# Optimization experiments

Hardware: AMD Instinct MI355X
Metric: run time of the kernel (lower is better)

The kernel has to match this reference:

```python
import jax, jax.numpy as jnp
import numpy as np

PATCH = 7
STRIDE = 1
PDIM = 3 * PATCH * PATCH  # 147


def _extract_patches(im):
    # torch.nn.Unfold(kernel=7, stride=1): output [b, c*k*k, L] with channel-major
    # ordering, which matches conv_general_dilated_patches' channel-major layout.
    b = im.shape[0]
    p = jax.lax.conv_general_dilated_patches(
        im, filter_shape=(PATCH, PATCH), window_strides=(STRIDE, STRIDE), padding='VALID'
    )  # [b, 147, h', w']
    p = p.reshape(b, PDIM, -1).transpose(0, 2, 1)  # [b, L, 147]
    # normalize_patch='mean': std_mean over ALL dims, only the mean is subtracted
    return p - p.mean()


def setup_inputs() -> dict:
    key = jax.random.key(0)
    k1, k2, k3, k4, k5 = jax.random.split(key, 5)
    B, C, H, W = 16, 3, 128, 128
    L = ((H - PATCH) // STRIDE + 1) ** 2  # 14884
    n_samples, n_proj = 4096, 128
    x = jax.random.normal(k1, (B, C, H, W), dtype=jnp.float32)
    y = jax.random.normal(k2, (B, C, H, W), dtype=jnp.float32)
    # faithful quirk: sample_same_locations=True re-draws a fresh permutation for y
    idx_x = jax.random.permutation(k3, L)[:n_samples].astype(jnp.int32)
    idx_y = jax.random.permutation(k4, L)[:n_samples].astype(jnp.int32)
    proj = jax.random.normal(k5, (PDIM, n_proj), dtype=jnp.float32)
    proj = proj / jnp.linalg.norm(proj, axis=0, keepdims=True)  # unit-norm slices
    return {"x": x, "y": y, "proj": proj, "idx_x": idx_x, "idx_y": idx_y}


def reference(x, y, proj, idx_x, idx_y):
    xp = _extract_patches(x)[:, idx_x]  # [b, n, 147]
    yp = _extract_patches(y)[:, idx_y]  # [b, n, 147]
    # SWD dist_metric, vectorized over the batch dim (replaces the Python loop):
    # project patches onto random unit directions, sort along the sample axis,
    # mean absolute difference of sorted projections.
    px = jnp.sort(jnp.einsum('bnd,dp->bnp', xp, proj), axis=1)  # [b, n, P]
    py = jnp.sort(jnp.einsum('bnd,dp->bnp', yp, proj), axis=1)
    per_sample = jnp.mean(jnp.abs(px - py), axis=(1, 2))  # [b]
    return per_sample.mean()  # batch_reduction='mean'
```

## Files before the change

### kernel.cpp

```cpp
#include <hip/hip_runtime.h>
#include <cstddef>
#include <cstdint>

#define BATCH 16
#define CHAN 3
#define HH 128
#define WW 128
#define PATCHK 7
#define HP 122
#define PDIM 147
#define NSAMP 4096
#define NPROJ 128
#define IMG_PIX (CHAN*HH*WW)
#define TOT_PIX (BATCH*IMG_PIX)
#define COUNT_D ((double)BATCH*HP*HP*PDIM)

__global__ __launch_bounds__(256)
void k_wsum(const float* __restrict__ x, const float* __restrict__ y,
            double* __restrict__ outx, double* __restrict__ outy) {
  float sx = 0.f, sy = 0.f;
  const int stride = gridDim.x * blockDim.x;
  for (int e = blockIdx.x * blockDim.x + threadIdx.x; e < TOT_PIX; e += stride) {
    int j = e & (WW - 1);
    int i = (e >> 7) & (HH - 1);
    int wi = min(i, HP - 1) - max(0, i - (PATCHK - 1)) + 1;
    int wj = min(j, HP - 1) - max(0, j - (PATCHK - 1)) + 1;
    float w = (float)(wi * wj);
    sx = fmaf(x[e], w, sx);
    sy = fmaf(y[e], w, sy);
  }
  __shared__ float rx[256], ry[256];
  const int tid = threadIdx.x;
  rx[tid] = sx; ry[tid] = sy;
  __syncthreads();
  for (int off = 128; off; off >>= 1) {
    if (tid < off) { rx[tid] += rx[tid + off]; ry[tid] += ry[tid + off]; }
    __syncthreads();
  }
  if (tid == 0) { outx[blockIdx.x] = (double)rx[0]; outy[blockIdx.x] = (double)ry[0]; }
}

__global__ void k_meandiff(const double* __restrict__ px, const double* __restrict__ py,
                           double* __restrict__ dmean,
                           const float* __restrict__ proj, float* __restrict__ sp) {
  const int tid = threadIdx.x;
  if (tid < NPROJ) {
    float s = 0.f;
    for (int d = 0; d < PDIM; ++d) s += proj[d * NPROJ + tid];
    sp[tid] = s;
  }
  __shared__ double sd[256];
  sd[tid] = px[tid] - py[tid];
  __syncthreads();
  for (int off = 128; off; off >>= 1) {
    if (tid < off) sd[tid] += sd[tid + off];
    __syncthreads();
  }
  if (tid == 0) dmean[0] = sd[0] / COUNT_D;
}

#define TM 64
#define ASTR (TM + 1)
__device__ __forceinline__ void loadb(float (&dst)[32], const float* bp, int kk) {
#pragma unroll
  for (int pp = 0; pp < 32; ++pp) dst[pp] = bp[kk * NPROJ + pp];
}
__device__ __forceinline__ void fma32(float a, const float (&b)[32], float (&acc)[32]) {
#pragma unroll
  for (int pp = 0; pp < 32; ++pp) acc[pp] = fmaf(a, b[pp], acc[pp]);
}

__global__ __launch_bounds__(256)
void k_proj(const float* __restrict__ x, const float* __restrict__ y,
            const float* __restrict__ proj,
            const int* __restrict__ idx_x, const int* __restrict__ idx_y,
            float* __restrict__ PX, float* __restrict__ PY) {
  __shared__ float As[PDIM * ASTR];

  const int z = blockIdx.z;
  const float* im = z ? y : x;
  const int* idx = z ? idx_y : idx_x;
  float* dst = z ? PY : PX;
  const int b = blockIdx.y;
  const int nbase = blockIdx.x * TM;
  const int tid = threadIdx.x;

  const float* imb = im + b * IMG_PIX;
  for (int e = tid; e < TM * PDIM; e += 256) {
    int n = e / PDIM;
    int d = e - n * PDIM;
    int l = idx[nbase + n];
    int h0 = l / HP;
    int w0 = l - h0 * HP;
    int c  = d / 49;
    int r  = d - c * 49;
    int kh = r / 7;
    int kw = r - kh * 7;
    As[d * ASTR + n] = imb[(c * HH + h0 + kh) * WW + w0 + kw];
  }
  __syncthreads();

  const int lane = tid & 63;
  const int w = __builtin_amdgcn_readfirstlane(tid >> 6);
  const float* bp = proj + w * 32;

  float acc[32];
#pragma unroll
  for (int pp = 0; pp < 32; ++pp) acc[pp] = 0.f;

  float bA[32], bB[32];
  loadb(bA, bp, 0);
  for (int k = 0; k + 2 < PDIM; k += 2) {
    loadb(bB, bp, k + 1);
    const float a0 = As[k * ASTR + lane];
    const float a1 = As[(k + 1) * ASTR + lane];
    fma32(a0, bA, acc);
    loadb(bA, bp, k + 2);
    fma32(a1, bB, acc);
  }
  {
    const float a = As[146 * ASTR + lane];
    fma32(a, bA, acc);
  }

#pragma unroll
  for (int pp = 0; pp < 32; ++pp)
    dst[(size_t)(b * NPROJ + w * 32 + pp) * NSAMP + nbase + lane] = acc[pp];
}

__device__ __forceinline__ float xorf(float v, unsigned m) {
  return __int_as_float(__float_as_int(v) ^ (int)m);
}
#define CSW(a, b) { float _t = fminf(a, b); b = fmaxf(a, b); a = _t; }

#define SORT8A(v) do { \
  CSW(v[0],v[1]); CSW(v[3],v[2]); CSW(v[4],v[5]); CSW(v[7],v[6]); \
  CSW(v[0],v[2]); CSW(v[1],v[3]); CSW(v[6],v[4]); CSW(v[7],v[5]); \
  CSW(v[0],v[1]); CSW(v[2],v[3]); CSW(v[5],v[4]); CSW(v[7],v[6]); \
  CSW(v[0],v[4]); CSW(v[1],v[5]); CSW(v[2],v[6]); CSW(v[3],v[7]); \
  CSW(v[0],v[2]); CSW(v[1],v[3]); CSW(v[4],v[6]); CSW(v[5],v[7]); \
  CSW(v[0],v[1]); CSW(v[2],v[3]); CSW(v[4],v[5]); CSW(v[6],v[7]); } while (0)

#define REG3A(v) do { \
  CSW(v[0],v[4]); CSW(v[1],v[5]); CSW(v[2],v[6]); CSW(v[3],v[7]); \
  CSW(v[0],v[2]); CSW(v[1],v[3]); CSW(v[4],v[6]); CSW(v[5],v[7]); \
  CSW(v[0],v[1]); CSW(v[2],v[3]); CSW(v[4],v[5]); CSW(v[6],v[7]); } while (0)

#define FLIP8(v, m) { v[0]=xorf(v[0],m); v[1]=xorf(v[1],m); v[2]=xorf(v[2],m); \
  v[3]=xorf(v[3],m); v[4]=xorf(v[4],m); v[5]=xorf(v[5],m); v[6]=xorf(v[6],m); \
  v[7]=xorf(v[7],m); }

template <int DL>
__device__ __forceinline__ float swzxor(float v) {
  if constexpr (DL <= 16) {
    return __int_as_float(
        __builtin_amdgcn_ds_swizzle(__float_as_int(v), (DL << 10) | 0x1F));
  } else {
    return __shfl_xor(v, DL, 64);
  }
}

template <int DL>
__device__ __forceinline__ void shufxy(float (&vx)[8], float (&vy)[8], bool keepLo) {
#pragma unroll
  for (int r = 0; r < 8; ++r) {
    float ox = swzxor<DL>(vx[r]);
    vx[r] = keepLo ? fminf(vx[r], ox) : fmaxf(vx[r], ox);
    float oy = swzxor<DL>(vy[r]);
    vy[r] = keepLo ? fminf(vy[r], oy) : fmaxf(vy[r], oy);
  }
}

__device__ __forceinline__ void lds_stage(float (&vx)[8], float (&vy)[8],
                                          float* lx, float* ly, int t, int dl, bool kl) {
  ((float4*)lx)[t * 2]     = make_float4(vx[0], vx[1], vx[2], vx[3]);
  ((float4*)lx)[t * 2 + 1] = make_float4(vx[4], vx[5], vx[6], vx[7]);
  ((float4*)ly)[t * 2]     = make_float4(vy[0], vy[1], vy[2], vy[3]);
  ((float4*)ly)[t * 2 + 1] = make_float4(vy[4], vy[5], vy[6], vy[7]);
  __syncthreads();
  const int pt = (t ^ dl) * 2;
  float4 ox0 = ((const float4*)lx)[pt], ox1 = ((const float4*)lx)[pt + 1];
  float4 oy0 = ((const float4*)ly)[pt], oy1 = ((const float4*)ly)[pt + 1];
  vx[0] = kl ? fminf(vx[0], ox0.x) : fmaxf(vx[0], ox0.x);
  vx[1] = kl ? fminf(vx[1], ox0.y) : fmaxf(vx[1], ox0.y);
  vx[2] = kl ? fminf(vx[2], ox0.z) : fmaxf(vx[2], ox0.z);
  vx[3] = kl ? fminf(vx[3], ox0.w) : fmaxf(vx[3], ox0.w);
  vx[4] = kl ? fminf(vx[4], ox1.x) : fmaxf(vx[4], ox1.x);
  vx[5] = kl ? fminf(vx[5], ox1.y) : fmaxf(vx[5], ox1.y);
  vx[6] = kl ? fminf(vx[6], ox1.z) : fmaxf(vx[6], ox1.z);
  vx[7] = kl ? fminf(vx[7], ox1.w) : fmaxf(vx[7], ox1.w);
  vy[0] = kl ? fminf(vy[0], oy0.x) : fmaxf(vy[0], oy0.x);
  vy[1] = kl ? fminf(vy[1], oy0.y) : fmaxf(vy[1], oy0.y);
  vy[2] = kl ? fminf(vy[2], oy0.z) : fmaxf(vy[2], oy0.z);
  vy[3] = kl ? fminf(vy[3], oy0.w) : fmaxf(vy[3], oy0.w);
  vy[4] = kl ? fminf(vy[4], oy1.x) : fmaxf(vy[4], oy1.x);
  vy[5] = kl ? fminf(vy[5], oy1.y) : fmaxf(vy[5], oy1.y);
  vy[6] = kl ? fminf(vy[6], oy1.z) : fmaxf(vy[6], oy1.z);
  vy[7] = kl ? fminf(vy[7], oy1.w) : fmaxf(vy[7], oy1.w);
  __syncthreads();
}

__global__ __launch_bounds__(512)
void k_sortdiff(const float* __restrict__ PX, const float* __restrict__ PY,
                const float* __restrict__ sp, const double* __restrict__ dmean,
                float* __restrict__ bsum) {
  __shared__ float lx[NSAMP];
  __shared__ float ly[NSAMP];
  __shared__ float red[8];
  const int bp = blockIdx.x;
  const int p = bp & (NPROJ - 1);
  const unsigned t = threadIdx.x;

  const unsigned g = t ^ (t >> 1);
  const unsigned mA    = (t & 1u)   << 31;
  const unsigned dA16  = (g & 1u)   << 31;
  const unsigned d16   = (g & 2u)   << 30;
  const unsigned d32   = (g & 4u)   << 29;
  const unsigned d64   = (g & 8u)   << 28;
  const unsigned d128  = (g & 16u)  << 27;
  const unsigned d256  = (g & 32u)  << 26;
  const unsigned d512  = (g & 64u)  << 25;
  const unsigned d1024 = (g & 128u) << 24;
  const unsigned d2048 = (t & 256u) << 23;

  const bool k1  = (t & 1u)  == 0, k2  = (t & 2u)  == 0, k4 = (t & 4u) == 0;
  const bool k8  = (t & 8u)  == 0, k16 = (t & 16u) == 0, k32 = (t & 32u) == 0;
  const bool kl64 = (t & 64u) == 0, kl128 = (t & 128u) == 0, kl256 = (t & 256u) == 0;

  float vx[8], vy[8];
  {
    const float4* rx = (const float4*)(PX + (size_t)bp * NSAMP) + t * 2;
    const float4* ry = (const float4*)(PY + (size_t)bp * NSAMP) + t * 2;
    float4 x0 = rx[0], x1 = rx[1], y0 = ry[0], y1 = ry[1];
    vx[0]=x0.x; vx[1]=x0.y; vx[2]=x0.z; vx[3]=x0.w;
    vx[4]=x1.x; vx[5]=x1.y; vx[6]=x1.z; vx[7]=x1.w;
    vy[0]=y0.x; vy[1]=y0.y; vy[2]=y0.z; vy[3]=y0.w;
    vy[4]=y1.x; vy[5]=y1.y; vy[6]=y1.z; vy[7]=y1.w;
  }

  FLIP8(vx, mA); FLIP8(vy, mA);
  SORT8A(vx); SORT8A(vy);
  FLIP8(vx, dA16); FLIP8(vy, dA16);

  shufxy<1>(vx, vy, k1); REG3A(vx); REG3A(vy);
  FLIP8(vx, d16); FLIP8(vy, d16);
  shufxy<2>(vx, vy, k2); shufxy<1>(vx, vy, k1); REG3A(vx); REG3A(vy);
  FLIP8(vx, d32); FLIP8(vy, d32);
  shufxy<4>(vx, vy, k4); shufxy<2>(vx, vy, k2); shufxy<1>(vx, vy, k1);
  REG3A(vx); REG3A(vy);
  FLIP8(vx, d64); FLIP8(vy, d64);
  shufxy<8>(vx, vy, k8); shufxy<4>(vx, vy, k4); shufxy<2>(vx, vy, k2);
  shufxy<1>(vx, vy, k1); REG3A(vx); REG3A(vy);
  FLIP8(vx, d128); FLIP8(vy, d128);
  shufxy<16>(vx, vy, k16); shufxy<8>(vx, vy, k8); shufxy<4>(vx, vy, k4);
  shufxy<2>(vx, vy, k2); shufxy<1>(vx, vy, k1); REG3A(vx); REG3A(vy);
  FLIP8(vx, d256); FLIP8(vy, d256);
  shufxy<32>(vx, vy, k32); shufxy<16>(vx, vy, k16); shufxy<8>(vx, vy, k8);
  shufxy<4>(vx, vy, k4); shufxy<2>(vx, vy, k2); shufxy<1>(vx, vy, k1);
  REG3A(vx); REG3A(vy);
  FLIP8(vx, d512); FLIP8(vy, d512);
  lds_stage(vx, vy, lx, ly, (int)t, 64, kl64);
  shufxy<32>(vx, vy, k32); shufxy<16>(vx, vy, k16); shufxy<8>(vx, vy, k8);
  shufxy<4>(vx, vy, k4); shufxy<2>(vx, vy, k2); shufxy<1>(vx, vy, k1);
  REG3A(vx); REG3A(vy);
  FLIP8(vx, d1024); FLIP8(vy, d1024);
  lds_stage(vx, vy, lx, ly, (int)t, 128, kl128);
  lds_stage(vx, vy, lx, ly, (int)t, 64, kl64);
  shufxy<32>(vx, vy, k32); shufxy<16>(vx, vy, k16); shufxy<8>(vx, vy, k8);
  shufxy<4>(vx, vy, k4); shufxy<2>(vx, vy, k2); shufxy<1>(vx, vy, k1);
  REG3A(vx); REG3A(vy);
  FLIP8(vx, d2048); FLIP8(vy, d2048);
  lds_stage(vx, vy, lx, ly, (int)t, 256, kl256);
  lds_stage(vx, vy, lx, ly, (int)t, 128, kl128);
  lds_stage(vx, vy, lx, ly, (int)t, 64, kl64);
  shufxy<32>(vx, vy, k32); shufxy<16>(vx, vy, k16); shufxy<8>(vx, vy, k8);
  shufxy<4>(vx, vy, k4); shufxy<2>(vx, vy, k2); shufxy<1>(vx, vy, k1);
  REG3A(vx); REG3A(vy);

  const float delta = (float)(dmean[0]) * sp[p];
  float s = 0.f;
#pragma unroll
  for (int r = 0; r < 8; ++r) s += fabsf(vx[r] - vy[r] - delta);

#pragma unroll
  for (int o = 1; o < 64; o <<= 1) s += __shfl_xor(s, o, 64);
  if ((t & 63u) == 0) red[t >> 6] = s;
  __syncthreads();
  if (t == 0) {
    float tot = 0.f;
#pragma unroll
    for (int i = 0; i < 8; ++i) tot += red[i];
    bsum[bp] = tot;
  }
}

__global__ void k_final(const float* __restrict__ bsum, float* __restrict__ out) {
  __shared__ double s[256];
  const int tid = threadIdx.x;
  double v = 0.0;
  for (int q = tid; q < BATCH * NPROJ; q += 256) v += (double)bsum[q];
  s[tid] = v;
  __syncthreads();
  for (int off = 128; off; off >>= 1) {
    if (tid < off) s[tid] += s[tid + off];
    __syncthreads();
  }
  if (tid == 0) out[0] = (float)(s[0] / ((double)NSAMP * NPROJ * BATCH));
}

extern "C" void kernel_launch(void* const* d_in, const int* in_sizes, int n_in,
                              void* d_out, int out_size, void* d_ws, size_t ws_size,
                              hipStream_t stream) {
  const float* x    = (const float*)d_in[0];
  const float* y    = (const float*)d_in[1];
  const float* proj = (const float*)d_in[2];
  const int* idx_x  = (const int*)d_in[3];
  const int* idx_y  = (const int*)d_in[4];
  float* out = (float*)d_out;

  char* ws = (char*)d_ws;
  double* pAx   = (double*)(ws + 0);
  double* pAy   = (double*)(ws + 2048);
  double* dmean = (double*)(ws + 4096);
  float*  sp    = (float*)(ws + 4160);
  float*  bsum  = (float*)(ws + 8192);
  float*  PX    = (float*)(ws + 16384);
  float*  PY    = PX + (size_t)BATCH * NPROJ * NSAMP;

  const size_t need = 16384 + 2ull * BATCH * NPROJ * NSAMP * sizeof(float);
  if (ws_size < need) return;

  k_wsum    <<<256, 256, 0, stream>>>(x, y, pAx, pAy);
  k_meandiff<<<1, 256, 0, stream>>>(pAx, pAy, dmean, proj, sp);
  k_proj    <<<dim3(NSAMP / TM, BATCH, 2), 256, 0, stream>>>(x, y, proj, idx_x, idx_y, PX, PY);
  k_sortdiff<<<BATCH * NPROJ, 512, 0, stream>>>(PX, PY, sp, dmean, bsum);
  k_final   <<<1, 256, 0, stream>>>(bsum, out);
}
```

Before: 251.1 us.

## Double per-thread sample tile in projection GEMM and precompute gather offsets

The projection kernel's sample tile grows from 64 to 128. Each lane now computes two samples, reading float2 from shared memory, so every proj value loaded is reused twice. The patch gather precomputes per-dimension and per-sample offsets in shared memory, replacing the per-element divisions. This halves the number of blocks and redundant proj loads, but doubles accumulator registers (64), which may lower occupancy.

```diff
diff --git a/kernel.cpp b/kernel.cpp
--- a/kernel.cpp
+++ b/kernel.cpp
@@ -59,15 +59,11 @@
   if (tid == 0) dmean[0] = sd[0] / COUNT_D;
 }
 
-#define TM 64
-#define ASTR (TM + 1)
+#define TM 128
+#define ASTR (TM + 2)
 __device__ __forceinline__ void loadb(float (&dst)[32], const float* bp, int kk) {
 #pragma unroll
   for (int pp = 0; pp < 32; ++pp) dst[pp] = bp[kk * NPROJ + pp];
-}
-__device__ __forceinline__ void fma32(float a, const float (&b)[32], float (&acc)[32]) {
-#pragma unroll
-  for (int pp = 0; pp < 32; ++pp) acc[pp] = fmaf(a, b[pp], acc[pp]);
 }
 
 __global__ __launch_bounds__(256)
@@ -76,6 +72,8 @@
             const int* __restrict__ idx_x, const int* __restrict__ idx_y,
             float* __restrict__ PX, float* __restrict__ PY) {
   __shared__ float As[PDIM * ASTR];
+  __shared__ int offd[PDIM];
+  __shared__ int basen[TM];
 
   const int z = blockIdx.z;
   const float* im = z ? y : x;
@@ -85,47 +83,65 @@
   const int nbase = blockIdx.x * TM;
   const int tid = threadIdx.x;
 
+  if (tid < PDIM) {
+    int c = tid / 49, r = tid - c * 49, kh = r / 7, kw = r - kh * 7;
+    offd[tid] = (c * HH + kh) * WW + kw;
+  }
+  if (tid < TM) {
+    int l = idx[nbase + tid];
+    int h0 = l / HP;
+    basen[tid] = h0 * WW + (l - h0 * HP);
+  }
+  __syncthreads();
+
   const float* imb = im + b * IMG_PIX;
-  for (int e = tid; e < TM * PDIM; e += 256) {
-    int n = e / PDIM;
-    int d = e - n * PDIM;
-    int l = idx[nbase + n];
-    int h0 = l / HP;
-    int w0 = l - h0 * HP;
-    int c  = d / 49;
-    int r  = d - c * 49;
-    int kh = r / 7;
-    int kw = r - kh * 7;
-    As[d * ASTR + n] = imb[(c * HH + h0 + kh) * WW + w0 + kw];
+  for (int q = tid; q < PDIM * TM; q += 256) {
+    int d = q >> 7;
+    int n = q & (TM - 1);
+    As[d * ASTR + n] = imb[basen[n] + offd[d]];
   }
   __syncthreads();
 
   const int lane = tid & 63;
   const int w = __builtin_amdgcn_readfirstlane(tid >> 6);
-  const float* bp = proj + w * 32;
-
-  float acc[32];
-#pragma unroll
-  for (int pp = 0; pp < 32; ++pp) acc[pp] = 0.f;
+  const float* bpr = proj + w * 32;
+
+  float acc0[32], acc1[32];
+#pragma unroll
+  for (int pp = 0; pp < 32; ++pp) { acc0[pp] = 0.f; acc1[pp] = 0.f; }
 
   float bA[32], bB[32];
-  loadb(bA, bp, 0);
+  loadb(bA, bpr, 0);
   for (int k = 0; k + 2 < PDIM; k += 2) {
-    loadb(bB, bp, k + 1);
-    const float a0 = As[k * ASTR + lane];
-    const float a1 = As[(k + 1) * ASTR + lane];
-    fma32(a0, bA, acc);
-    loadb(bA, bp, k + 2);
-    fma32(a1, bB, acc);
+    loadb(bB, bpr, k + 1);
+    const float2 a0 = *(const float2*)&As[k * ASTR + lane * 2];
+    const float2 a1 = *(const float2*)&As[(k + 1) * ASTR + lane * 2];
+#pragma unroll
+    for (int pp = 0; pp < 32; ++pp) {
+      acc0[pp] = fmaf(a0.x, bA[pp], acc0[pp]);
+      acc1[pp] = fmaf(a0.y, bA[pp], acc1[pp]);
+    }
+    loadb(bA, bpr, k + 2);
+#pragma unroll
+    for (int pp = 0; pp < 32; ++pp) {
+      acc0[pp] = fmaf(a1.x, bB[pp], acc0[pp]);
+      acc1[pp] = fmaf(a1.y, bB[pp], acc1[pp]);
+    }
   }
   {
-    const float a = As[146 * ASTR + lane];
-    fma32(a, bA, acc);
-  }
-
-#pragma unroll
-  for (int pp = 0; pp < 32; ++pp)
-    dst[(size_t)(b * NPROJ + w * 32 + pp) * NSAMP + nbase + lane] = acc[pp];
+    const float2 a = *(const float2*)&As[146 * ASTR + lane * 2];
+#pragma unroll
+    for (int pp = 0; pp < 32; ++pp) {
+      acc0[pp] = fmaf(a.x, bA[pp], acc0[pp]);
+      acc1[pp] = fmaf(a.y, bA[pp], acc1[pp]);
+    }
+  }
+
+#pragma unroll
+  for (int pp = 0; pp < 32; ++pp) {
+    float* o = dst + (size_t)(b * NPROJ + w * 32 + pp) * NSAMP + nbase + lane * 2;
+    *(float2*)o = make_float2(acc0[pp], acc1[pp]);
+  }
 }
 
 __device__ __forceinline__ float xorf(float v, unsigned m) {
```

Result: slower. 270.2 us (+7.6%).
